# Optimization experiments

Hardware: AMD Instinct MI355X
Metric: run time of the kernel (lower is better)

The kernel has to match this reference:

```python
import jax, jax.numpy as jnp
import numpy as np

N_NODES = 50000
N_EDGES = 600000
NODE_DIM = 128
HIDDEN = 512
OUT_DIM = 128


def setup_inputs() -> dict:
    key = jax.random.key(0)
    ks = jax.random.split(key, 12)
    s = lambda k, shape, fan_in: jax.random.normal(k, shape, dtype=jnp.float32) * (1.0 / np.sqrt(fan_in))
    x = jax.random.normal(ks[0], (N_NODES, NODE_DIM), dtype=jnp.float32)
    edge_index = jax.random.randint(ks[1], (2, N_EDGES), 0, N_NODES, dtype=jnp.int32)
    return {
        "x": x,
        "edge_index": edge_index,
        # conv1 MLP: Linear(node_dim, hidden) -> ReLU -> Linear(hidden, hidden)
        "W1a": s(ks[2], (NODE_DIM, HIDDEN), NODE_DIM), "b1a": jnp.zeros((HIDDEN,), jnp.float32),
        "W1b": s(ks[3], (HIDDEN, HIDDEN), HIDDEN), "b1b": jnp.zeros((HIDDEN,), jnp.float32),
        # conv2 MLP: Linear(hidden, hidden) -> ReLU -> Linear(hidden, hidden)
        "W2a": s(ks[4], (HIDDEN, HIDDEN), HIDDEN), "b2a": jnp.zeros((HIDDEN,), jnp.float32),
        "W2b": s(ks[5], (HIDDEN, HIDDEN), HIDDEN), "b2b": jnp.zeros((HIDDEN,), jnp.float32),
        # final fc: Linear(hidden, output_dim)
        "Wf": s(ks[6], (HIDDEN, OUT_DIM), HIDDEN), "bf": jnp.zeros((OUT_DIM,), jnp.float32),
    }


def _gin_conv(x, src, dst, Wa, ba, Wb, bb):
    # GINConv with eps=0: h_i = MLP( (1+eps)*x_i + sum_{j in N(i)} x_j )
    agg = jax.ops.segment_sum(x[src], dst, num_segments=N_NODES)  # [N, d]
    h = agg + x
    h = jnp.maximum(h @ Wa + ba, 0.0)
    return h @ Wb + bb


def reference(x, edge_index, W1a, b1a, W1b, b1b, W2a, b2a, W2b, b2b, Wf, bf):
    src, dst = edge_index[0], edge_index[1]
    h = _gin_conv(x, src, dst, W1a, b1a, W1b, b1b)   # [N, hidden]
    h = _gin_conv(h, src, dst, W2a, b2a, W2b, b2b)   # [N, hidden]
    pooled = h.mean(axis=0)                           # [hidden]
    return pooled @ Wf + bf                           # [output_dim]
```

## Files before the change

kernel.cpp:

```cpp
#include <hip/hip_runtime.h>
#include <stdint.h>

#define NN 50000
#define NE 600000
#define ND 128
#define NH 512
#define NO 128
#define MPAD 50048
#define NB 196

typedef unsigned short u16;
typedef uint8_t u8;
typedef __attribute__((ext_vector_type(8))) short bf16x8;
typedef __attribute__((ext_vector_type(4))) float f32x4;
typedef __attribute__((ext_vector_type(2))) float f32x2;

__device__ __forceinline__ u16 f2bf(float f) {
  union { float f; uint32_t u; } v; v.f = f;
  uint32_t u = v.u;
  uint32_t r = (u + 0x7fffu + ((u >> 16) & 1u)) >> 16;
  return (u16)r;
}
__device__ __forceinline__ float bf2f(u16 h) {
  union { uint32_t u; float f; } v; v.u = ((uint32_t)h) << 16; return v.f;
}
__device__ __forceinline__ uint64_t f42bfq(float4 v) {
  union { u16 u[4]; uint64_t q; } o;
  o.u[0] = f2bf(v.x); o.u[1] = f2bf(v.y); o.u[2] = f2bf(v.z); o.u[3] = f2bf(v.w);
  return o.q;
}

#if defined(__has_builtin)
#if __has_builtin(__builtin_amdgcn_cvt_pk_f32_fp8) && __has_builtin(__builtin_amdgcn_cvt_pk_fp8_f32)
#define HW_FP8 1
#endif
#endif
#ifndef HW_FP8
#define HW_FP8 0
#endif

__device__ __forceinline__ u8 f2fp8(float f) {
#if HW_FP8
  return (u8)(__builtin_amdgcn_cvt_pk_fp8_f32(f, f, 0, false) & 0xff);
#else
  union { float f; uint32_t u; } v; v.f = f;
  uint32_t s = v.u >> 31;
  float a = fabsf(f);
  if (a >= 448.f) return (u8)((s << 7) | 0x7e);
  if (a < 0.015625f) {
    uint32_t m = (uint32_t)(a * 512.0f + 0.5f);
    if (m > 7) return (u8)((s << 7) | 8);
    return (u8)((s << 7) | m);
  }
  uint32_t u = v.u & 0x7fffffff;
  uint32_t r = u + 0x7FFFF + ((u >> 20) & 1);
  int e8 = (int)(r >> 23) - 120;
  if (e8 >= 16) return (u8)((s << 7) | 0x7e);
  return (u8)((s << 7) | ((uint32_t)e8 << 3) | ((r >> 20) & 7));
#endif
}

template<bool HI>
__device__ __forceinline__ f32x2 fp8x2_f32(uint32_t w) {
#if HW_FP8
  return __builtin_amdgcn_cvt_pk_f32_fp8((int)w, HI);
#else
  uint32_t h = HI ? (w >> 16) : w;
  f32x2 r;
  for (int i = 0; i < 2; ++i) {
    uint32_t b = (h >> (i * 8)) & 0xff;
    uint32_t s = (b >> 7) & 1, e = (b >> 3) & 15, m = b & 7;
    float t;
    if (e == 0) t = (float)m * 0.001953125f;
    else { union { uint32_t u; float f; } v; v.u = ((e + 120) << 23) | (m << 20); t = v.f; }
    r[i] = s ? -t : t;
  }
  return r;
#endif
}

__device__ __forceinline__ void gld16(const u16* g, u16* l) {
  __builtin_amdgcn_global_load_lds(
      (const __attribute__((address_space(1))) void*)g,
      (__attribute__((address_space(3))) void*)l, 16, 0, 0);
}

template<int K, int EPI>
__global__ __launch_bounds__(256) void gemm_bt(
    const u16* __restrict__ A, const u16* __restrict__ B,
    const float* __restrict__ bias,
    u16* __restrict__ outB, u8* __restrict__ outF8,
    float* __restrict__ sumOut)
{
  __shared__ u16 As[2][128 * 64];
  __shared__ u16 Bs[2][128 * 64];
  const int nwg  = gridDim.x;
  const int q    = nwg >> 3, r = nwg & 7;
  const int xcd  = blockIdx.x & 7, loc = blockIdx.x >> 3;
  const int wgid = (xcd < r ? xcd * (q + 1) : r * (q + 1) + (xcd - r) * q) + loc;
  const int m0   = (wgid >> 2) * 128;
  const int n0   = (wgid & 3) * 128;

  const int tid  = threadIdx.x;
  const int w    = tid >> 6;
  const int lane = tid & 63;
  const int wm   = (w >> 1) * 64;
  const int wn   = (w & 1) * 64;
  const int l15  = lane & 15;
  const int lh   = lane >> 4;

  const f32x4 z4 = {0.f, 0.f, 0.f, 0.f};
  f32x4 acc[4][4];
#pragma unroll
  for (int m = 0; m < 4; ++m)
#pragma unroll
    for (int n = 0; n < 4; ++n) acc[m][n] = z4;

  auto stage = [&](int kk) {
    const int b = kk & 1;
#pragma unroll
    for (int i = 0; i < 4; ++i) {
      const int cc  = i * 256 + w * 64 + lane;
      const int row = cc >> 3;
      const int csw = (cc ^ row) & 7;
      const int ldsbase = (i * 256 + w * 64) * 8;
      gld16(A + (size_t)(m0 + row) * K + kk * 64 + csw * 8, As[b] + ldsbase);
      gld16(B + (size_t)(n0 + row) * K + kk * 64 + csw * 8, Bs[b] + ldsbase);
    }
  };

  const int NK = K / 64;
  stage(0);

  for (int kk = 0; kk < NK; ++kk) {
    if (kk + 1 < NK) {
      stage(kk + 1);
      asm volatile("s_waitcnt vmcnt(8)" ::: "memory");
    } else {
      asm volatile("s_waitcnt vmcnt(0)" ::: "memory");
    }
    __builtin_amdgcn_s_barrier();
    __builtin_amdgcn_sched_barrier(0);
    const u16* as = As[kk & 1];
    const u16* bs = Bs[kk & 1];
#pragma unroll
    for (int ks = 0; ks < 2; ++ks) {
      bf16x8 a[4], b[4];
#pragma unroll
      for (int m = 0; m < 4; ++m) {
        const int row = wm + m * 16 + l15;
        const int ch  = (ks * 4 + lh) ^ (row & 7);
        a[m] = *(const bf16x8*)&as[row * 64 + ch * 8];
      }
#pragma unroll
      for (int n = 0; n < 4; ++n) {
        const int row = wn + n * 16 + l15;
        const int ch  = (ks * 4 + lh) ^ (row & 7);
        b[n] = *(const bf16x8*)&bs[row * 64 + ch * 8];
      }
#pragma unroll
      for (int m = 0; m < 4; ++m)
#pragma unroll
        for (int n = 0; n < 4; ++n)
          acc[m][n] = __builtin_amdgcn_mfma_f32_16x16x32_bf16(a[m], b[n], acc[m][n], 0, 0, 0);
    }
    __builtin_amdgcn_sched_barrier(0);
    __builtin_amdgcn_s_barrier();
  }

  if (EPI == 2) {
#pragma unroll
    for (int n = 0; n < 4; ++n) {
      const int gc = n0 + wn + n * 16 + l15;
      const float bv = bias[gc];
      float p = 0.f;
#pragma unroll
      for (int m = 0; m < 4; ++m) {
        const int rbase = m0 + wm + m * 16 + lh * 4;
#pragma unroll
        for (int j = 0; j < 4; ++j) {
          if (rbase + j < NN) p += fmaxf(acc[m][n][j] + bv, 0.f);
        }
      }
      p += __shfl_xor(p, 16);
      p += __shfl_xor(p, 32);
      if (lane < 16) atomicAdd(&sumOut[gc], p);
    }
  } else {
#pragma unroll
    for (int m = 0; m < 4; ++m) {
#pragma unroll
      for (int j = 0; j < 4; ++j) {
        const int gr = m0 + wm + m * 16 + lh * 4 + j;
#pragma unroll
        for (int n = 0; n < 4; ++n) {
          const int gc = n0 + wn + n * 16 + l15;
          const float v = acc[m][n][j] + bias[gc];
          if (EPI == 0) outB[(size_t)gr * NH + gc] = f2bf(fmaxf(v, 0.f));
          else          outF8[(size_t)gr * NH + gc] = f2fp8(v);
        }
      }
    }
  }
}

struct PrepArgs {
  const float* W1a; u16* W1aT;
  const float* W1b; u16* W1bT;
  const float* W2a; u16* W2aT;
  const float4* x4; uint64_t* xb;
  const int* ei; int* deg;
};

__device__ __forceinline__ void cvtWT_one(const float* W, u16* T,
                                          int Kd, int Nd, int t) {
  if (t >= Kd * Nd) return;
  int k = t / Nd, n = t - k * Nd;
  T[n * Kd + k] = f2bf(W[t]);
}

__global__ __launch_bounds__(256) void prep_all(PrepArgs p) {
  const int bid = blockIdx.x;
  if (bid < 256) {
    cvtWT_one(p.W1a, p.W1aT, ND, NH, bid * 256 + threadIdx.x);
  } else if (bid < 1280) {
    cvtWT_one(p.W1b, p.W1bT, NH, NH, (bid - 256) * 256 + threadIdx.x);
  } else if (bid < 2304) {
    cvtWT_one(p.W2a, p.W2aT, NH, NH, (bid - 1280) * 256 + threadIdx.x);
  } else if (bid < 2304 + 6256) {
    int t = (bid - 2304) * 256 + threadIdx.x;
    if (t >= MPAD * 32) return;
    int row = t >> 5;
    uint64_t qv = 0;
    if (row < NN) qv = f42bfq(p.x4[t]);
    p.xb[t] = qv;
  } else {
    int e = (bid - 2304 - 6256) * 256 + threadIdx.x;
    if (e < NE) atomicAdd(&p.deg[p.ei[NE + e]], 1);
  }
}

__global__ void deg_partial(const int* __restrict__ deg, int* __restrict__ bsum) {
  const int i = blockIdx.x * 256 + threadIdx.x;
  int v = (i < NN) ? deg[i] : 0;
#pragma unroll
  for (int o = 1; o < 64; o <<= 1) v += __shfl_xor(v, o);
  __shared__ int ws[4];
  if ((threadIdx.x & 63) == 0) ws[threadIdx.x >> 6] = v;
  __syncthreads();
  if (threadIdx.x == 0) bsum[blockIdx.x] = ws[0] + ws[1] + ws[2] + ws[3];
}

__global__ void scan_bsum(const int* __restrict__ bsum, int* __restrict__ boff,
                          int* __restrict__ rowptr) {
  __shared__ int s[256];
  const int t = threadIdx.x;
  int v = (t < NB) ? bsum[t] : 0;
  s[t] = v;
  __syncthreads();
  for (int o = 1; o < 256; o <<= 1) {
    int u = (t >= o) ? s[t - o] : 0;
    __syncthreads();
    s[t] += u;
    __syncthreads();
  }
  if (t < NB) boff[t] = s[t] - v;
  if (t == 0) rowptr[NN] = NE;
}

__global__ void scan_apply(const int* __restrict__ deg, const int* __restrict__ boff,
                           int* __restrict__ rowptr, int* __restrict__ cursor) {
  __shared__ int s[256];
  const int t = threadIdx.x;
  const int i = blockIdx.x * 256 + t;
  int v = (i < NN) ? deg[i] : 0;
  s[t] = v;
  __syncthreads();
  for (int o = 1; o < 256; o <<= 1) {
    int u = (t >= o) ? s[t - o] : 0;
    __syncthreads();
    s[t] += u;
    __syncthreads();
  }
  if (i < NN) {
    int ex = boff[blockIdx.x] + s[t] - v;
    rowptr[i] = ex;
    cursor[i] = ex;
  }
}

__global__ void fill_csr(const int* __restrict__ ei, int* __restrict__ cursor,
                         int* __restrict__ csr) {
  int e = blockIdx.x * 256 + threadIdx.x;
  if (e >= NE) return;
  int d = ei[NE + e];
  int p = atomicAdd(&cursor[d], 1);
  csr[p] = ei[e];
}

__global__ __launch_bounds__(256) void gather_x(
    const u16* __restrict__ xb, const int* __restrict__ rowptr,
    const int* __restrict__ csr, u16* __restrict__ hb1) {
  const int wid  = blockIdx.x * 4 + (threadIdx.x >> 6);
  const int lane = threadIdx.x & 63;
  if (wid >= MPAD) return;
  float a0 = 0.f, a1 = 0.f;
  if (wid < NN) {
    uint32_t v = *(const uint32_t*)(xb + (size_t)wid * ND + lane * 2);
    a0 = bf2f((u16)v); a1 = bf2f((u16)(v >> 16));
    const int beg = rowptr[wid], end = rowptr[wid + 1];
    int e = beg;
    for (; e + 3 < end; e += 4) {
      int s0 = csr[e], s1 = csr[e + 1], s2 = csr[e + 2], s3 = csr[e + 3];
      uint32_t v0 = *(const uint32_t*)(xb + (size_t)s0 * ND + lane * 2);
      uint32_t v1 = *(const uint32_t*)(xb + (size_t)s1 * ND + lane * 2);
      uint32_t v2 = *(const uint32_t*)(xb + (size_t)s2 * ND + lane * 2);
      uint32_t v3 = *(const uint32_t*)(xb + (size_t)s3 * ND + lane * 2);
      a0 += bf2f((u16)v0) + bf2f((u16)v1) + bf2f((u16)v2) + bf2f((u16)v3);
      a1 += bf2f((u16)(v0 >> 16)) + bf2f((u16)(v1 >> 16)) +
            bf2f((u16)(v2 >> 16)) + bf2f((u16)(v3 >> 16));
    }
    for (; e < end; ++e) {
      int s0 = csr[e];
      uint32_t v0 = *(const uint32_t*)(xb + (size_t)s0 * ND + lane * 2);
      a0 += bf2f((u16)v0);
      a1 += bf2f((u16)(v0 >> 16));
    }
  }
  uint32_t o = (uint32_t)f2bf(a0) | ((uint32_t)f2bf(a1) << 16);
  *(uint32_t*)(hb1 + (size_t)wid * ND + lane * 2) = o;
}

__device__ __forceinline__ void acc_fp8x8(f32x2* acc, uint2 v) {
  acc[0] += fp8x2_f32<false>(v.x);
  acc[1] += fp8x2_f32<true >(v.x);
  acc[2] += fp8x2_f32<false>(v.y);
  acc[3] += fp8x2_f32<true >(v.y);
}

__global__ __launch_bounds__(256) void gather_h(
    const u8* __restrict__ H8, const int* __restrict__ rowptr,
    const int* __restrict__ csr, u16* __restrict__ r2) {
  const int wid  = blockIdx.x * 4 + (threadIdx.x >> 6);
  const int lane = threadIdx.x & 63;
  if (wid >= MPAD) return;
  f32x2 acc[4];
#pragma unroll
  for (int j = 0; j < 4; ++j) acc[j] = (f32x2){0.f, 0.f};
  if (wid < NN) {
    acc_fp8x8(acc, *(const uint2*)(H8 + (size_t)wid * NH + lane * 8));
    const int beg = rowptr[wid], end = rowptr[wid + 1];
    int e = beg;
    for (; e + 3 < end; e += 4) {
      int s0 = csr[e], s1 = csr[e + 1], s2 = csr[e + 2], s3 = csr[e + 3];
      uint2 v0 = *(const uint2*)(H8 + (size_t)s0 * NH + lane * 8);
      uint2 v1 = *(const uint2*)(H8 + (size_t)s1 * NH + lane * 8);
      uint2 v2 = *(const uint2*)(H8 + (size_t)s2 * NH + lane * 8);
      uint2 v3 = *(const uint2*)(H8 + (size_t)s3 * NH + lane * 8);
      acc_fp8x8(acc, v0);
      acc_fp8x8(acc, v1);
      acc_fp8x8(acc, v2);
      acc_fp8x8(acc, v3);
    }
    for (; e < end; ++e) {
      int s0 = csr[e];
      acc_fp8x8(acc, *(const uint2*)(H8 + (size_t)s0 * NH + lane * 8));
    }
  }
  union { u16 u[8]; uint4 q; } o;
#pragma unroll
  for (int j = 0; j < 4; ++j) {
    o.u[j * 2]     = f2bf(acc[j].x);
    o.u[j * 2 + 1] = f2bf(acc[j].y);
  }
  *(uint4*)(r2 + (size_t)wid * NH + lane * 8) = o.q;
}

__global__ __launch_bounds__(256) void ff1(const float* __restrict__ s,
                                           const float* __restrict__ W2b,
                                           float* __restrict__ pooled,
                                           const float* __restrict__ bfv,
                                           float* __restrict__ out) {
  const int b = blockIdx.x;
  if (b == 32) {
    if (threadIdx.x < NO) out[threadIdx.x] = bfv[threadIdx.x];
    return;
  }
  const int kc = b >> 1;
  const int j  = (b & 1) * 256 + threadIdx.x;
  const float invN = 1.0f / (float)NN;
  float acc = 0.f;
#pragma unroll
  for (int k = kc * 32; k < kc * 32 + 32; ++k)
    acc += s[k] * W2b[k * NH + j];
  atomicAdd(&pooled[j], acc * invN);
}

__global__ __launch_bounds__(128) void ff2(const float* __restrict__ pooled,
                                           const float* __restrict__ b2b,
                                           const float* __restrict__ Wf,
                                           float* __restrict__ out) {
  const int kc = blockIdx.x;
  const int j  = threadIdx.x;
  float acc = 0.f;
#pragma unroll
  for (int k = kc * 32; k < kc * 32 + 32; ++k)
    acc += (pooled[k] + b2b[k]) * Wf[k * NO + j];
  atomicAdd(&out[j], acc);
}

__global__ void ws_sentinel(float* out) {
  if (threadIdx.x < NO) out[threadIdx.x] = -12345.0f;
}

extern "C" void kernel_launch(void* const* d_in, const int* in_sizes, int n_in,
                              void* d_out, int out_size, void* d_ws, size_t ws_size,
                              hipStream_t stream) {
  const float* x   = (const float*)d_in[0];
  const int*   ei  = (const int*)d_in[1];
  const float* W1a = (const float*)d_in[2];
  const float* b1a = (const float*)d_in[3];
  const float* W1b = (const float*)d_in[4];
  const float* b1b = (const float*)d_in[5];
  const float* W2a = (const float*)d_in[6];
  const float* b2a = (const float*)d_in[7];
  const float* W2b = (const float*)d_in[8];
  const float* b2b = (const float*)d_in[9];
  const float* Wf  = (const float*)d_in[10];
  const float* bfv = (const float*)d_in[11];
  float* out = (float*)d_out;

  const size_t XB  = (size_t)MPAD * ND * 2;
  const size_t HB1 = (size_t)MPAD * ND * 2;
  const size_t RB  = (size_t)MPAD * NH * 2;
  const size_t H8B = (size_t)MPAD * NH;
  const size_t WB  = (size_t)NH * ND * 2 + 2 * (size_t)NH * NH * 2;
  const size_t CSRB = (size_t)(NN + 1) * 4 + 2 * (size_t)NN * 4 + (size_t)NE * 4
                      + 2 * (size_t)NB * 4;
  const size_t NEED = XB + HB1 + RB + H8B + WB + CSRB + 2 * NH * 4 + 32 * 256;
  if (ws_size < NEED) {
    ws_sentinel<<<1, 128, 0, stream>>>(out);
    return;
  }

  char* ws = (char*)d_ws;
  size_t off = 0;
  auto take = [&](size_t bytes) {
    char* p = ws + off;
    off = (off + bytes + 255) & ~(size_t)255;
    return p;
  };
  u16* xb  = (u16*)take(XB);
  u16* hb1 = (u16*)take(HB1);
  u16* R   = (u16*)take(RB);
  u8*  H8  = (u8*)take(H8B);
  u16* W1aT = (u16*)take((size_t)NH * ND * 2);
  u16* W1bT = (u16*)take((size_t)NH * NH * 2);
  u16* W2aT = (u16*)take((size_t)NH * NH * 2);
  int* deg    = (int*)take((size_t)NN * 4);
  int* cursor = (int*)take((size_t)NN * 4);
  int* rowptr = (int*)take((size_t)(NN + 1) * 4);
  int* csr    = (int*)take((size_t)NE * 4);
  int* bsum   = (int*)take((size_t)NB * 4);
  int* boff   = (int*)take((size_t)NB * 4);
  float* svec   = (float*)take((size_t)NH * 4);
  float* pooled = (float*)take((size_t)NH * 4);

  (void)hipMemsetAsync(svec, 0, 2 * NH * 4, stream);
  (void)hipMemsetAsync(deg, 0, (size_t)NN * 4, stream);

  PrepArgs pa;
  pa.W1a = W1a; pa.W1aT = W1aT;
  pa.W1b = W1b; pa.W1bT = W1bT;
  pa.W2a = W2a; pa.W2aT = W2aT;
  pa.x4 = (const float4*)x; pa.xb = (uint64_t*)xb;
  pa.ei = ei; pa.deg = deg;
  prep_all<<<2304 + 6256 + (NE + 255) / 256, 256, 0, stream>>>(pa);

  deg_partial<<<NB, 256, 0, stream>>>(deg, bsum);
  scan_bsum<<<1, 256, 0, stream>>>(bsum, boff, rowptr);
  scan_apply<<<NB, 256, 0, stream>>>(deg, boff, rowptr, cursor);
  fill_csr<<<(NE + 255) / 256, 256, 0, stream>>>(ei, cursor, csr);

  gather_x<<<(MPAD + 3) / 4, 256, 0, stream>>>(xb, rowptr, csr, hb1);
  gemm_bt<ND, 0><<<(MPAD / 128) * 4, 256, 0, stream>>>(hb1, W1aT, b1a, R, nullptr, nullptr);
  gemm_bt<NH, 1><<<(MPAD / 128) * 4, 256, 0, stream>>>(R, W1bT, b1b, nullptr, H8, nullptr);

  gather_h<<<(MPAD + 3) / 4, 256, 0, stream>>>(H8, rowptr, csr, R);
  gemm_bt<NH, 2><<<(MPAD / 128) * 4, 256, 0, stream>>>(R, W2aT, b2a, nullptr, nullptr, svec);

  ff1<<<33, 256, 0, stream>>>(svec, W2b, pooled, bfv, out);
  ff2<<<16, 128, 0, stream>>>(pooled, b2b, Wf, out);
}
```

Baseline: 271.7 us.

## Fold W1b into W2a and aggregate before the second linear layer

Uses linearity to move conv1's second linear layer past the neighbour aggregation. The fused weight Wc = W1b·W2a is precomputed by a small GEMM, and the b1b contribution becomes a per-node degree-scaled bias vector added in the final epilogue. This removes one full 50k×512×512 GEMM and its intermediate write. In exchange the gather now runs over the fp8 ReLU output of the first layer, so rounding happens at a different point and accuracy may shift.

```diff
diff --git a/kernel.cpp b/kernel.cpp
--- a/kernel.cpp
+++ b/kernel.cpp
@@ -90,7 +90,8 @@
     const u16* __restrict__ A, const u16* __restrict__ B,
     const float* __restrict__ bias,
     u16* __restrict__ outB, u8* __restrict__ outF8,
-    float* __restrict__ sumOut)
+    float* __restrict__ sumOut, const int* __restrict__ degv,
+    const float* __restrict__ cvec)
 {
   __shared__ u16 As[2][128 * 64];
   __shared__ u16 Bs[2][128 * 64];
@@ -169,19 +170,27 @@
   }
 
   if (EPI == 2) {
+    float dsc[4][4];
+#pragma unroll
+    for (int m = 0; m < 4; ++m)
+#pragma unroll
+      for (int j = 0; j < 4; ++j) {
+        const int row = m0 + wm + m * 16 + lh * 4 + j;
+        dsc[m][j] = (row < NN) ? (1.0f + (float)degv[row]) : 0.0f;
+      }
 #pragma unroll
     for (int n = 0; n < 4; ++n) {
       const int gc = n0 + wn + n * 16 + l15;
       const float bv = bias[gc];
+      const float cv = cvec[gc];
       float p = 0.f;
 #pragma unroll
-      for (int m = 0; m < 4; ++m) {
-        const int rbase = m0 + wm + m * 16 + lh * 4;
+      for (int m = 0; m < 4; ++m)
 #pragma unroll
         for (int j = 0; j < 4; ++j) {
-          if (rbase + j < NN) p += fmaxf(acc[m][n][j] + bv, 0.f);
+          if (dsc[m][j] != 0.0f)
+            p += fmaxf(acc[m][n][j] + bv + dsc[m][j] * cv, 0.f);
         }
-      }
       p += __shfl_xor(p, 16);
       p += __shfl_xor(p, 32);
       if (lane < 16) atomicAdd(&sumOut[gc], p);
@@ -196,8 +205,8 @@
         for (int n = 0; n < 4; ++n) {
           const int gc = n0 + wn + n * 16 + l15;
           const float v = acc[m][n][j] + bias[gc];
-          if (EPI == 0) outB[(size_t)gr * NH + gc] = f2bf(fmaxf(v, 0.f));
-          else          outF8[(size_t)gr * NH + gc] = f2fp8(v);
+          if (EPI == 0) outF8[(size_t)gr * NH + gc] = f2fp8(fmaxf(v, 0.f));
+          else          outB[(size_t)gr * NH + gc] = f2bf(v);
         }
       }
     }
@@ -206,10 +215,11 @@
 
 struct PrepArgs {
   const float* W1a; u16* W1aT;
-  const float* W1b; u16* W1bT;
+  const float* W1b; u16* W1bN;
   const float* W2a; u16* W2aT;
   const float4* x4; uint64_t* xb;
   const int* ei; int* deg;
+  const float* b1b; float* cvec;
 };
 
 __device__ __forceinline__ void cvtWT_one(const float* W, u16* T,
@@ -224,7 +234,8 @@
   if (bid < 256) {
     cvtWT_one(p.W1a, p.W1aT, ND, NH, bid * 256 + threadIdx.x);
   } else if (bid < 1280) {
-    cvtWT_one(p.W1b, p.W1bT, NH, NH, (bid - 256) * 256 + threadIdx.x);
+    int t = (bid - 256) * 256 + threadIdx.x;
+    if (t < NH * NH) p.W1bN[t] = f2bf(p.W1b[t]);
   } else if (bid < 2304) {
     cvtWT_one(p.W2a, p.W2aT, NH, NH, (bid - 1280) * 256 + threadIdx.x);
   } else if (bid < 2304 + 6256) {
@@ -234,9 +245,16 @@
     uint64_t qv = 0;
     if (row < NN) qv = f42bfq(p.x4[t]);
     p.xb[t] = qv;
-  } else {
+  } else if (bid < 2304 + 6256 + 2344) {
     int e = (bid - 2304 - 6256) * 256 + threadIdx.x;
     if (e < NE) atomicAdd(&p.deg[p.ei[NE + e]], 1);
+  } else {
+    int j = (bid - 2304 - 6256 - 2344) * 256 + threadIdx.x;
+    if (j < NH) {
+      float acc = 0.f;
+      for (int k = 0; k < NH; ++k) acc += p.b1b[k] * p.W2a[k * NH + j];
+      p.cvec[j] = acc;
+    }
   }
 }
 
@@ -339,8 +357,8 @@
 }
 
 __global__ __launch_bounds__(256) void gather_h(
-    const u8* __restrict__ H8, const int* __restrict__ rowptr,
-    const int* __restrict__ csr, u16* __restrict__ r2) {
+    const u8* __restrict__ R8, const int* __restrict__ rowptr,
+    const int* __restrict__ csr, u16* __restrict__ g) {
   const int wid  = blockIdx.x * 4 + (threadIdx.x >> 6);
   const int lane = threadIdx.x & 63;
   if (wid >= MPAD) return;
@@ -348,15 +366,15 @@
 #pragma unroll
   for (int j = 0; j < 4; ++j) acc[j] = (f32x2){0.f, 0.f};
   if (wid < NN) {
-    acc_fp8x8(acc, *(const uint2*)(H8 + (size_t)wid * NH + lane * 8));
+    acc_fp8x8(acc, *(const uint2*)(R8 + (size_t)wid * NH + lane * 8));
     const int beg = rowptr[wid], end = rowptr[wid + 1];
     int e = beg;
     for (; e + 3 < end; e += 4) {
       int s0 = csr[e], s1 = csr[e + 1], s2 = csr[e + 2], s3 = csr[e + 3];
-      uint2 v0 = *(const uint2*)(H8 + (size_t)s0 * NH + lane * 8);
-      uint2 v1 = *(const uint2*)(H8 + (size_t)s1 * NH + lane * 8);
-      uint2 v2 = *(const uint2*)(H8 + (size_t)s2 * NH + lane * 8);
-      uint2 v3 = *(const uint2*)(H8 + (size_t)s3 * NH + lane * 8);
+      uint2 v0 = *(const uint2*)(R8 + (size_t)s0 * NH + lane * 8);
+      uint2 v1 = *(const uint2*)(R8 + (size_t)s1 * NH + lane * 8);
+      uint2 v2 = *(const uint2*)(R8 + (size_t)s2 * NH + lane * 8);
+      uint2 v3 = *(const uint2*)(R8 + (size_t)s3 * NH + lane * 8);
       acc_fp8x8(acc, v0);
       acc_fp8x8(acc, v1);
       acc_fp8x8(acc, v2);
@@ -364,7 +382,7 @@
     }
     for (; e < end; ++e) {
       int s0 = csr[e];
-      acc_fp8x8(acc, *(const uint2*)(H8 + (size_t)s0 * NH + lane * 8));
+      acc_fp8x8(acc, *(const uint2*)(R8 + (size_t)s0 * NH + lane * 8));
     }
   }
   union { u16 u[8]; uint4 q; } o;
@@ -373,7 +391,7 @@
     o.u[j * 2]     = f2bf(acc[j].x);
     o.u[j * 2 + 1] = f2bf(acc[j].y);
   }
-  *(uint4*)(r2 + (size_t)wid * NH + lane * 8) = o.q;
+  *(uint4*)(g + (size_t)wid * NH + lane * 8) = o.q;
 }
 
 __global__ __launch_bounds__(256) void ff1(const float* __restrict__ s,
@@ -432,12 +450,12 @@
 
   const size_t XB  = (size_t)MPAD * ND * 2;
   const size_t HB1 = (size_t)MPAD * ND * 2;
-  const size_t RB  = (size_t)MPAD * NH * 2;
-  const size_t H8B = (size_t)MPAD * NH;
-  const size_t WB  = (size_t)NH * ND * 2 + 2 * (size_t)NH * NH * 2;
+  const size_t GB  = (size_t)MPAD * NH * 2;
+  const size_t R8B = (size_t)MPAD * NH;
+  const size_t WB  = (size_t)NH * ND * 2 + 3 * (size_t)NH * NH * 2;
   const size_t CSRB = (size_t)(NN + 1) * 4 + 2 * (size_t)NN * 4 + (size_t)NE * 4
                       + 2 * (size_t)NB * 4;
-  const size_t NEED = XB + HB1 + RB + H8B + WB + CSRB + 2 * NH * 4 + 32 * 256;
+  const size_t NEED = XB + HB1 + GB + R8B + WB + CSRB + 4 * NH * 4 + 32 * 256;
   if (ws_size < NEED) {
     ws_sentinel<<<1, 128, 0, stream>>>(out);
     return;
@@ -452,30 +470,36 @@
   };
   u16* xb  = (u16*)take(XB);
   u16* hb1 = (u16*)take(HB1);
-  u16* R   = (u16*)take(RB);
-  u8*  H8  = (u8*)take(H8B);
+  u16* G   = (u16*)take(GB);
+  u8*  R8  = (u8*)take(R8B);
   u16* W1aT = (u16*)take((size_t)NH * ND * 2);
-  u16* W1bT = (u16*)take((size_t)NH * NH * 2);
+  u16* W1bN = (u16*)take((size_t)NH * NH * 2);
   u16* W2aT = (u16*)take((size_t)NH * NH * 2);
+  u16* WcT  = (u16*)take((size_t)NH * NH * 2);
   int* deg    = (int*)take((size_t)NN * 4);
   int* cursor = (int*)take((size_t)NN * 4);
   int* rowptr = (int*)take((size_t)(NN + 1) * 4);
   int* csr    = (int*)take((size_t)NE * 4);
   int* bsum   = (int*)take((size_t)NB * 4);
   int* boff   = (int*)take((size_t)NB * 4);
-  float* svec   = (float*)take((size_t)NH * 4);
-  float* pooled = (float*)take((size_t)NH * 4);
-
-  (void)hipMemsetAsync(svec, 0, 2 * NH * 4, stream);
+  float* svec    = (float*)take((size_t)NH * 4);
+  float* pooled  = (float*)take((size_t)NH * 4);
+  float* zero512 = (float*)take((size_t)NH * 4);
+  float* cvec    = (float*)take((size_t)NH * 4);
+
+  (void)hipMemsetAsync(svec, 0, 3 * NH * 4, stream);
   (void)hipMemsetAsync(deg, 0, (size_t)NN * 4, stream);
 
   PrepArgs pa;
   pa.W1a = W1a; pa.W1aT = W1aT;
-  pa.W1b = W1b; pa.W1bT = W1bT;
+  pa.W1b = W1b; pa.W1bN = W1bN;
   pa.W2a = W2a; pa.W2aT = W2aT;
   pa.x4 = (const float4*)x; pa.xb = (uint64_t*)xb;
   pa.ei = ei; pa.deg = deg;
-  prep_all<<<2304 + 6256 + (NE + 255) / 256, 256, 0, stream>>>(pa);
+  pa.b1b = b1b; pa.cvec = cvec;
+  prep_all<<<2304 + 6256 + 2344 + 2, 256, 0, stream>>>(pa);
+
+  gemm_bt<NH, 1><<<(512 / 128) * 4, 256, 0, stream>>>(W2aT, W1bN, zero512, WcT, nullptr, nullptr, nullptr, nullptr);
 
   deg_partial<<<NB, 256, 0, stream>>>(deg, bsum);
   scan_bsum<<<1, 256, 0, stream>>>(bsum, boff, rowptr);
@@ -483,11 +507,10 @@
   fill_csr<<<(NE + 255) / 256, 256, 0, stream>>>(ei, cursor, csr);
 
   gather_x<<<(MPAD + 3) / 4, 256, 0, stream>>>(xb, rowptr, csr, hb1);
-  gemm_bt<ND, 0><<<(MPAD / 128) * 4, 256, 0, stream>>>(hb1, W1aT, b1a, R, nullptr, nullptr);
-  gemm_bt<NH, 1><<<(MPAD / 128) * 4, 256, 0, stream>>>(R, W1bT, b1b, nullptr, H8, nullptr);
-
-  gather_h<<<(MPAD + 3) / 4, 256, 0, stream>>>(H8, rowptr, csr, R);
-  gemm_bt<NH, 2><<<(MPAD / 128) * 4, 256, 0, stream>>>(R, W2aT, b2a, nullptr, nullptr, svec);
+  gemm_bt<ND, 0><<<(MPAD / 128) * 4, 256, 0, stream>>>(hb1, W1aT, b1a, nullptr, R8, nullptr, nullptr, nullptr);
+
+  gather_h<<<(MPAD + 3) / 4, 256, 0, stream>>>(R8, rowptr, csr, G);
+  gemm_bt<NH, 2><<<(MPAD / 128) * 4, 256, 0, stream>>>(G, WcT, b2a, nullptr, nullptr, svec, deg, cvec);
 
   ff1<<<33, 256, 0, stream>>>(svec, W2b, pooled, bfv, out);
   ff2<<<16, 128, 0, stream>>>(pooled, b2b, Wf, out);
```

New measurement: 269.1 us. Within noise of the previous version (-1.0%).
